# Performance work log

Hardware: AMD Instinct MI355X
Metric: run time of the kernel (lower is better)

Reference implementation:

```python
import jax, jax.numpy as jnp
import numpy as np
from jax import lax

NUM_STEPS = 32
NUM_CLASSES = 10
HIDDEN = 1024


def setup_inputs() -> dict:
    key = jax.random.key(0)
    ks = jax.random.split(key, 4)
    B, H, W, C = 8, 1024, 2048, 4
    x = jax.random.normal(ks[0], (B, H, W, C), dtype=jnp.float32)
    conv_w = jax.random.normal(ks[1], (C,), dtype=jnp.float32) * 0.5
    conv_b = jnp.zeros((1,), dtype=jnp.float32)
    w1 = jax.random.normal(ks[2], (HIDDEN, W), dtype=jnp.float32) * (1.0 / np.sqrt(W))
    b1 = jnp.zeros((HIDDEN,), dtype=jnp.float32)
    w2 = jax.random.normal(ks[3], (NUM_CLASSES, HIDDEN), dtype=jnp.float32) * (1.0 / np.sqrt(HIDDEN))
    b2 = jnp.zeros((NUM_CLASSES,), dtype=jnp.float32)
    beta1 = jnp.full((1,), 0.95, dtype=jnp.float32)
    thr1 = jnp.ones((1,), dtype=jnp.float32)
    beta2 = jnp.full((1,), 0.95, dtype=jnp.float32)
    thr2 = jnp.ones((1,), dtype=jnp.float32)
    return {"x": x, "conv_w": conv_w, "conv_b": conv_b, "w1": w1, "b1": b1,
            "beta1": beta1, "thr1": thr1, "w2": w2, "b2": b2,
            "beta2": beta2, "thr2": thr2}


def _leaky_scan(inp_t, beta, thr):
    # inp_t: [T, ...]; snntorch Leaky, reset_mechanism='subtract', reset_delay=False
    b = jnp.clip(beta, 0.0, 1.0)

    def step(mem, u):
        mem = b * mem + u
        spk = (mem > thr).astype(u.dtype)   # heaviside spike
        mem = mem - spk * thr               # subtract reset (no delay)
        return mem, spk

    mem0 = jnp.zeros(inp_t.shape[1:], dtype=inp_t.dtype)
    _, spks = lax.scan(step, mem0, inp_t)
    return spks  # [T, ...]


def reference(x, conv_w, conv_b, w1, b1, beta1, thr1, w2, b2, beta2, thr2):
    # x: [B, H, W, 4]; 1x1 conv over 4 antenna channels -> 1 channel
    xf = jnp.einsum('bhwc,c->bhw', x, conv_w) + conv_b[0]       # [B, H, W]
    B, H, W = xf.shape
    G = H // NUM_STEPS
    xr = xf.reshape(B, G, NUM_STEPS, W)                          # [B, G, T, 2048]
    h = jnp.einsum('bgtw,dw->bgtd', xr, w1) + b1                 # [B, G, T, D]
    spks1 = _leaky_scan(jnp.moveaxis(h, 2, 0), beta1, thr1)      # [T, B, G, D]
    s = spks1.sum(axis=0)                                        # [B, G, D]
    h2 = jnp.einsum('bgd,cd->bgc', s, w2) + b2                   # [B, G, C]
    spks2 = _leaky_scan(jnp.moveaxis(h2, 1, 0), beta2, thr2)     # [G, B, C]
    logits = spks2.sum(axis=0)                                   # [B, C]
    return jax.nn.softmax(logits, axis=1)
```

## Files before the change

kernel.cpp:

```cpp
#include <hip/hip_runtime.h>

#define TSTEPS 32
#define HID 1024
#define NCLS 10
#define BATCH 8
#define GGRP 32
#define MROWS 8192
#define GK 2048
#define GN 1024
#define BUFSH 24576

typedef __attribute__((ext_vector_type(8))) short bf16x8;
typedef __attribute__((ext_vector_type(16))) float f32x16;

__device__ __forceinline__ unsigned short bf16_rne(float v) {
    unsigned u = __builtin_bit_cast(unsigned, v);
    return (unsigned short)((u + 0x7FFFu + ((u >> 16) & 1u)) >> 16);
}
__device__ __forceinline__ float bf16_f(unsigned short h) {
    unsigned u = (unsigned)h << 16;
    return __builtin_bit_cast(float, u);
}
__device__ __forceinline__ void gload16(const unsigned short* g, unsigned short* l) {
    __builtin_amdgcn_global_load_lds(
        (const __attribute__((address_space(1))) void*)g,
        (__attribute__((address_space(3))) void*)l, 16, 0, 0);
}


__global__ __launch_bounds__(256) void conv_pack_kernel(
    const float4* __restrict__ x, const float* __restrict__ cw,
    const float* __restrict__ cb,
    unsigned short* __restrict__ Ahi, unsigned short* __restrict__ Alo)
{
    const int rb = blockIdx.x >> 6;
    const int kb = blockIdx.x & 63;
    const float c0 = cw[0], c1 = cw[1], c2 = cw[2], c3 = cw[3], cbv = cb[0];
    const int tid = threadIdx.x;
#pragma unroll
    for (int cc = 0; cc < 2; ++cc) {
        int c = tid + cc * 256;
        int u = c >> 6, w = c & 63;
        int row = (u >> 1) * 32 + (w & 31);
        int k0  = (u & 1) * 16 + (w >> 5) * 8;
        const float4* px = x + ((size_t)(rb * 128 + row) * 2048 + kb * 32 + k0);
        bf16x8 h8, l8;
#pragma unroll
        for (int e = 0; e < 8; ++e) {
            float4 a = px[e];
            float v = a.x * c0 + a.y * c1 + a.z * c2 + a.w * c3 + cbv;
            unsigned short h = bf16_rne(v);
            h8[e] = (short)h;
            l8[e] = (short)bf16_rne(v - bf16_f(h));
        }
        size_t off = ((size_t)blockIdx.x * 512 + c) * 8;
        *(bf16x8*)(Ahi + off) = h8;
        *(bf16x8*)(Alo + off) = l8;
    }
}

__global__ __launch_bounds__(256) void wpack_kernel(
    const float* __restrict__ wsrc, unsigned short* __restrict__ Bhi,
    unsigned short* __restrict__ Blo)
{
    const int kb  = blockIdx.x & 63;
    const int cbk = blockIdx.x >> 6;
    const int tid = threadIdx.x;
#pragma unroll
    for (int cc = 0; cc < 4; ++cc) {
        int c = tid + cc * 256;
        int u = c >> 6, w = c & 63;
        int col = cbk * 256 + (u >> 1) * 32 + (w & 31);
        int k0  = kb * 32 + (u & 1) * 16 + (w >> 5) * 8;
        const float* pw = wsrc + ((size_t)col * 2048 + k0);
        bf16x8 h8, l8;
#pragma unroll
        for (int e = 0; e < 8; ++e) {
            float v = pw[e];
            unsigned short h = bf16_rne(v);
            h8[e] = (short)h;
            l8[e] = (short)bf16_rne(v - bf16_f(h));
        }
        size_t off = ((size_t)blockIdx.x * 1024 + c) * 8;
        *(bf16x8*)(Bhi + off) = h8;
        *(bf16x8*)(Blo + off) = l8;
    }
}

__global__ __launch_bounds__(512) void gemm_scan_kernel(
    const unsigned short* __restrict__ Ahi, const unsigned short* __restrict__ Alo,
    const unsigned short* __restrict__ Bhi, const unsigned short* __restrict__ Blo,
    const float* __restrict__ bias,
    const float* __restrict__ beta1, const float* __restrict__ thr1,
    float* __restrict__ S)
{
    __shared__ __align__(16) unsigned short sm[3 * BUFSH];

    const int tid = threadIdx.x;
    const int lane = tid & 63, wv = tid >> 6;
    const int wr = wv >> 2, wc = wv & 3;
    const int by = blockIdx.x & 63;
    const int bx = blockIdx.x >> 6;

    const unsigned short* gAh = Ahi + (size_t)by * 262144;
    const unsigned short* gAl = Alo + (size_t)by * 262144;
    const unsigned short* gBh = Bhi + (size_t)bx * 524288;
    const unsigned short* gBl = Blo + (size_t)bx * 524288;

    f32x16 acc[2][2];
#pragma unroll
    for (int i = 0; i < 2; ++i)
#pragma unroll
        for (int j = 0; j < 2; ++j) acc[i][j] = (f32x16)0.f;

#define STAGE(buf, kb_)                                                          \
    {                                                                            \
        unsigned short* dst = sm + (buf) * BUFSH;                                \
        const size_t ao = (size_t)(kb_) * 4096 + tid * 8;                        \
        const size_t bo = (size_t)(kb_) * 8192 + tid * 8;                        \
        gload16(gAh + ao, dst + tid * 8);                                        \
        gload16(gAl + ao, dst + 4096 + tid * 8);                                 \
        gload16(gBh + bo, dst + 8192 + tid * 8);                                 \
        gload16(gBh + bo + 4096, dst + 12288 + tid * 8);                         \
        gload16(gBl + bo, dst + 16384 + tid * 8);                                \
        gload16(gBl + bo + 4096, dst + 20480 + tid * 8);                         \
    }

    STAGE(0, 0);
    STAGE(1, 1);

    const int fo = ((lane & 31) + 32 * (lane >> 5)) * 8;

    int cur = 0;
    for (int kb = 0; kb < 64; ++kb) {
        if (kb < 63) asm volatile("s_waitcnt vmcnt(6)" ::: "memory");
        else         asm volatile("s_waitcnt vmcnt(0)" ::: "memory");
        __builtin_amdgcn_s_barrier();

        int nbuf = cur + 2; if (nbuf >= 3) nbuf -= 3;
        if (kb < 62) STAGE(nbuf, kb + 2);

        const unsigned short* bufp = sm + cur * BUFSH;
        bf16x8 ah[2][2], al[2][2], bh[2][2], bl[2][2];
#pragma unroll
        for (int i = 0; i < 2; ++i)
#pragma unroll
            for (int kh = 0; kh < 2; ++kh) {
                int ua = (((wr * 2 + i) * 2 + kh) << 9) + fo;
                ah[i][kh] = *(const bf16x8*)(bufp + ua);
                al[i][kh] = *(const bf16x8*)(bufp + 4096 + ua);
            }
#pragma unroll
        for (int j = 0; j < 2; ++j)
#pragma unroll
            for (int kh = 0; kh < 2; ++kh) {
                int ub = (((wc * 2 + j) * 2 + kh) << 9) + fo;
                bh[j][kh] = *(const bf16x8*)(bufp + 8192 + ub);
                bl[j][kh] = *(const bf16x8*)(bufp + 16384 + ub);
            }
#pragma unroll
        for (int kh = 0; kh < 2; ++kh) {
#pragma unroll
            for (int i = 0; i < 2; ++i)
#pragma unroll
                for (int j = 0; j < 2; ++j)
                    acc[i][j] = __builtin_amdgcn_mfma_f32_32x32x16_bf16(ah[i][kh], bh[j][kh], acc[i][j], 0, 0, 0);
#pragma unroll
            for (int i = 0; i < 2; ++i)
#pragma unroll
                for (int j = 0; j < 2; ++j)
                    acc[i][j] = __builtin_amdgcn_mfma_f32_32x32x16_bf16(ah[i][kh], bl[j][kh], acc[i][j], 0, 0, 0);
#pragma unroll
            for (int i = 0; i < 2; ++i)
#pragma unroll
                for (int j = 0; j < 2; ++j)
                    acc[i][j] = __builtin_amdgcn_mfma_f32_32x32x16_bf16(al[i][kh], bh[j][kh], acc[i][j], 0, 0, 0);
        }
        cur = (cur == 2) ? 0 : cur + 1;
    }
    __syncthreads();

    float* sb = (float*)sm;
    const float bclamp = fminf(fmaxf(beta1[0], 0.f), 1.f);
    const float th = thr1[0];
    const int sbg = tid >> 8;
    const int scol = tid & 255;
    const float bv = bias[bx * 256 + scol];

#pragma unroll
    for (int band = 0; band < 2; ++band) {
        if (wr == band) {
#pragma unroll
            for (int i = 0; i < 2; ++i)
#pragma unroll
                for (int j = 0; j < 2; ++j)
#pragma unroll
                    for (int r = 0; r < 16; ++r) {
                        int lr = i * 32 + (r & 3) + 8 * (r >> 2) + 4 * (lane >> 5);
                        int lc = wc * 64 + j * 32 + (lane & 31);
                        sb[lr * 256 + lc] = acc[i][j][r];
                    }
        }
        __syncthreads();
        float mem = 0.f, cnt = 0.f;
#pragma unroll
        for (int t = 0; t < TSTEPS; ++t) {
            float u = sb[(sbg * 32 + t) * 256 + scol] + bv;
            mem = bclamp * mem + u;
            float spk = mem > th ? 1.f : 0.f;
            mem -= spk * th;
            cnt += spk;
        }
        int bgg = by * 4 + band * 2 + sbg;
        S[(size_t)bgg * GN + bx * 256 + scol] = cnt;
        __syncthreads();
    }
}

__global__ __launch_bounds__(256) void fc2_kernel(
    const float* __restrict__ s, const float* __restrict__ w2,
    const float* __restrict__ b2, float* __restrict__ h2)
{
    int bg  = blockIdx.x;
    int tid = threadIdx.x;
    const float* sp = s + (size_t)bg * HID;
    float part[NCLS];
#pragma unroll
    for (int c = 0; c < NCLS; ++c) part[c] = 0.f;
    for (int d = tid; d < HID; d += 256) {
        float sv = sp[d];
#pragma unroll
        for (int c = 0; c < NCLS; ++c) part[c] += sv * w2[c * HID + d];
    }
#pragma unroll
    for (int c = 0; c < NCLS; ++c)
        for (int off = 32; off > 0; off >>= 1)
            part[c] += __shfl_down(part[c], off, 64);
    __shared__ float red[NCLS][4];
    int wave = tid >> 6, lanei = tid & 63;
    if (lanei == 0)
#pragma unroll
        for (int c = 0; c < NCLS; ++c) red[c][wave] = part[c];
    __syncthreads();
    if (tid < NCLS) {
        float v = red[tid][0] + red[tid][1] + red[tid][2] + red[tid][3] + b2[tid];
        h2[bg * NCLS + tid] = v;
    }
}

__global__ __launch_bounds__(128) void scan2_kernel(
    const float* __restrict__ h2, const float* __restrict__ beta2,
    const float* __restrict__ thr2, float* __restrict__ out)
{
    __shared__ float logits[BATCH][NCLS];
    int t = threadIdx.x;
    if (t < BATCH * NCLS) {
        int b = t / NCLS, c = t % NCLS;
        float bb = fminf(fmaxf(beta2[0], 0.f), 1.f);
        float th = thr2[0];
        float mem = 0.f, lg = 0.f;
        for (int g = 0; g < GGRP; ++g) {
            float u = h2[(b * GGRP + g) * NCLS + c];
            mem = bb * mem + u;
            float spk = mem > th ? 1.f : 0.f;
            mem -= spk * th;
            lg += spk;
        }
        logits[b][c] = lg;
    }
    __syncthreads();
    if (t < BATCH) {
        float mx = -1e30f;
        for (int c = 0; c < NCLS; ++c) mx = fmaxf(mx, logits[t][c]);
        float e[NCLS];
        float sum = 0.f;
        for (int c = 0; c < NCLS; ++c) { e[c] = expf(logits[t][c] - mx); sum += e[c]; }
        for (int c = 0; c < NCLS; ++c) out[t * NCLS + c] = e[c] / sum;
    }
}

extern "C" void kernel_launch(void* const* d_in, const int* in_sizes, int n_in,
                              void* d_out, int out_size, void* d_ws, size_t ws_size,
                              hipStream_t stream)
{
    const float* x     = (const float*)d_in[0];
    const float* cw    = (const float*)d_in[1];
    const float* cb    = (const float*)d_in[2];
    const float* w1    = (const float*)d_in[3];
    const float* b1    = (const float*)d_in[4];
    const float* beta1 = (const float*)d_in[5];
    const float* thr1  = (const float*)d_in[6];
    const float* w2    = (const float*)d_in[7];
    const float* b2    = (const float*)d_in[8];
    const float* beta2 = (const float*)d_in[9];
    const float* thr2  = (const float*)d_in[10];
    float* out = (float*)d_out;

    unsigned short* ahi = (unsigned short*)d_ws;
    unsigned short* alo = ahi + (size_t)MROWS * GK;
    unsigned short* bhi = alo + (size_t)MROWS * GK;
    unsigned short* blo = bhi + (size_t)GN * GK;
    float* s  = (float*)(blo + (size_t)GN * GK);
    float* h2 = s + (size_t)BATCH * GGRP * HID;

    conv_pack_kernel<<<4096, 256, 0, stream>>>((const float4*)x, cw, cb, ahi, alo);
    wpack_kernel    <<<256, 256, 0, stream>>>(w1, bhi, blo);
    gemm_scan_kernel<<<256, 512, 0, stream>>>(ahi, alo, bhi, blo, b1, beta1, thr1, s);
    fc2_kernel      <<<256, 256, 0, stream>>>(s, w2, b2, h2);
    scan2_kernel    <<<1, 128, 0, stream>>>(h2, beta2, thr2, out);
}
```

Baseline: 171.6 us.

## Coalesce conv-pack loads via LDS and software-pipeline GEMM fragment reads

The conv/pack kernel now reads x with coalesced float4 loads, so consecutive threads read consecutive pixels. It converts the values to bf16 hi/lo pairs in a padded LDS tile and then writes the packed fragments from LDS, replacing the old per-thread strided 8-pixel loads. In the GEMM kernel the main loop is unrolled by two, with double-buffered register fragments. LDS reads for the next k-block are issued before the MFMAs of the current one, and the prologue prefetches three stages. This is meant to hide LDS latency behind MFMA work and cut DRAM inefficiency in the bandwidth-bound conv stage, at the cost of more registers and extra LDS in the pack kernel.

```diff
diff --git a/kernel.cpp b/kernel.cpp
--- a/kernel.cpp
+++ b/kernel.cpp
@@ -9,6 +9,7 @@
 #define GK 2048
 #define GN 1024
 #define BUFSH 24576
+#define CLDS 40
 
 typedef __attribute__((ext_vector_type(8))) short bf16x8;
 typedef __attribute__((ext_vector_type(16))) float f32x16;
@@ -33,26 +34,33 @@
     const float* __restrict__ cb,
     unsigned short* __restrict__ Ahi, unsigned short* __restrict__ Alo)
 {
+    __shared__ __align__(16) unsigned short lh[128 * CLDS];
+    __shared__ __align__(16) unsigned short ll[128 * CLDS];
     const int rb = blockIdx.x >> 6;
     const int kb = blockIdx.x & 63;
     const float c0 = cw[0], c1 = cw[1], c2 = cw[2], c3 = cw[3], cbv = cb[0];
     const int tid = threadIdx.x;
+
+#pragma unroll
+    for (int p = 0; p < 16; ++p) {
+        int i = p * 256 + tid;
+        int row = i >> 5, px = i & 31;
+        float4 a = x[(size_t)(rb * 128 + row) * 2048 + kb * 32 + px];
+        float v = a.x * c0 + a.y * c1 + a.z * c2 + a.w * c3 + cbv;
+        unsigned short h = bf16_rne(v);
+        lh[row * CLDS + px] = h;
+        ll[row * CLDS + px] = bf16_rne(v - bf16_f(h));
+    }
+    __syncthreads();
+
 #pragma unroll
     for (int cc = 0; cc < 2; ++cc) {
         int c = tid + cc * 256;
         int u = c >> 6, w = c & 63;
         int row = (u >> 1) * 32 + (w & 31);
-        int k0  = (u & 1) * 16 + (w >> 5) * 8;
-        const float4* px = x + ((size_t)(rb * 128 + row) * 2048 + kb * 32 + k0);
-        bf16x8 h8, l8;
-#pragma unroll
-        for (int e = 0; e < 8; ++e) {
-            float4 a = px[e];
-            float v = a.x * c0 + a.y * c1 + a.z * c2 + a.w * c3 + cbv;
-            unsigned short h = bf16_rne(v);
-            h8[e] = (short)h;
-            l8[e] = (short)bf16_rne(v - bf16_f(h));
-        }
+        int ko  = (u & 1) * 2 + (w >> 5);
+        bf16x8 h8 = *(const bf16x8*)(lh + row * CLDS + ko * 8);
+        bf16x8 l8 = *(const bf16x8*)(ll + row * CLDS + ko * 8);
         size_t off = ((size_t)blockIdx.x * 512 + c) * 8;
         *(bf16x8*)(Ahi + off) = h8;
         *(bf16x8*)(Alo + off) = l8;
@@ -112,6 +120,8 @@
     for (int i = 0; i < 2; ++i)
 #pragma unroll
         for (int j = 0; j < 2; ++j) acc[i][j] = (f32x16)0.f;
+
+    bf16x8 fr[2][16];
 
 #define STAGE(buf, kb_)                                                          \
     {                                                                            \
@@ -126,58 +136,83 @@
         gload16(gBl + bo + 4096, dst + 20480 + tid * 8);                         \
     }
 
+#define READF(s, bufp)                                                           \
+    {                                                                            \
+        const unsigned short* bp_ = (bufp);                                      \
+        _Pragma("unroll")                                                        \
+        for (int i = 0; i < 2; ++i)                                              \
+            _Pragma("unroll")                                                    \
+            for (int kh = 0; kh < 2; ++kh) {                                     \
+                int ua = (((wr * 2 + i) * 2 + kh) << 9) + fo;                    \
+                fr[s][(i * 2 + kh) * 2 + 0] = *(const bf16x8*)(bp_ + ua);        \
+                fr[s][(i * 2 + kh) * 2 + 1] = *(const bf16x8*)(bp_ + 4096 + ua); \
+            }                                                                    \
+        _Pragma("unroll")                                                        \
+        for (int j = 0; j < 2; ++j)                                              \
+            _Pragma("unroll")                                                    \
+            for (int kh = 0; kh < 2; ++kh) {                                     \
+                int ub = (((wc * 2 + j) * 2 + kh) << 9) + fo;                    \
+                fr[s][8 + (j * 2 + kh) * 2 + 0] = *(const bf16x8*)(bp_ + 8192 + ub);  \
+                fr[s][8 + (j * 2 + kh) * 2 + 1] = *(const bf16x8*)(bp_ + 16384 + ub); \
+            }                                                                    \
+    }
+
+#define MFMAF(s)                                                                 \
+    {                                                                            \
+        _Pragma("unroll")                                                        \
+        for (int kh = 0; kh < 2; ++kh) {                                         \
+            _Pragma("unroll")                                                    \
+            for (int i = 0; i < 2; ++i)                                          \
+                _Pragma("unroll")                                                \
+                for (int j = 0; j < 2; ++j)                                      \
+                    acc[i][j] = __builtin_amdgcn_mfma_f32_32x32x16_bf16(         \
+                        fr[s][(i * 2 + kh) * 2], fr[s][8 + (j * 2 + kh) * 2],    \
+                        acc[i][j], 0, 0, 0);                                     \
+            _Pragma("unroll")                                                    \
+            for (int i = 0; i < 2; ++i)                                          \
+                _Pragma("unroll")                                                \
+                for (int j = 0; j < 2; ++j)                                      \
+                    acc[i][j] = __builtin_amdgcn_mfma_f32_32x32x16_bf16(         \
+                        fr[s][(i * 2 + kh) * 2], fr[s][8 + (j * 2 + kh) * 2 + 1],\
+                        acc[i][j], 0, 0, 0);                                     \
+            _Pragma("unroll")                                                    \
+            for (int i = 0; i < 2; ++i)                                          \
+                _Pragma("unroll")                                                \
+                for (int j = 0; j < 2; ++j)                                      \
+                    acc[i][j] = __builtin_amdgcn_mfma_f32_32x32x16_bf16(         \
+                        fr[s][(i * 2 + kh) * 2 + 1], fr[s][8 + (j * 2 + kh) * 2],\
+                        acc[i][j], 0, 0, 0);                                     \
+        }                                                                        \
+    }
+
+#define KSTEP(SC, SN, KB)                                                        \
+    {                                                                            \
+        if ((KB) < 63) asm volatile("s_waitcnt vmcnt(6)" ::: "memory");          \
+        else           asm volatile("s_waitcnt vmcnt(0)" ::: "memory");          \
+        asm volatile("s_waitcnt lgkmcnt(0)" ::: "memory");                       \
+        __builtin_amdgcn_sched_barrier(0);                                       \
+        __builtin_amdgcn_s_barrier();                                            \
+        if ((KB) <= 61) STAGE(((KB) + 2) % 3, (KB) + 2);                         \
+        READF(SN, sm + ((KB) % 3) * BUFSH);                                      \
+        MFMAF(SC);                                                               \
+    }
+
     STAGE(0, 0);
     STAGE(1, 1);
-
+    STAGE(2, 2);
+    asm volatile("s_waitcnt vmcnt(12)" ::: "memory");
+    __builtin_amdgcn_s_barrier();
     const int fo = ((lane & 31) + 32 * (lane >> 5)) * 8;
-
-    int cur = 0;
-    for (int kb = 0; kb < 64; ++kb) {
-        if (kb < 63) asm volatile("s_waitcnt vmcnt(6)" ::: "memory");
-        else         asm volatile("s_waitcnt vmcnt(0)" ::: "memory");
-        __builtin_amdgcn_s_barrier();
-
-        int nbuf = cur + 2; if (nbuf >= 3) nbuf -= 3;
-        if (kb < 62) STAGE(nbuf, kb + 2);
-
-        const unsigned short* bufp = sm + cur * BUFSH;
-        bf16x8 ah[2][2], al[2][2], bh[2][2], bl[2][2];
-#pragma unroll
-        for (int i = 0; i < 2; ++i)
-#pragma unroll
-            for (int kh = 0; kh < 2; ++kh) {
-                int ua = (((wr * 2 + i) * 2 + kh) << 9) + fo;
-                ah[i][kh] = *(const bf16x8*)(bufp + ua);
-                al[i][kh] = *(const bf16x8*)(bufp + 4096 + ua);
-            }
-#pragma unroll
-        for (int j = 0; j < 2; ++j)
-#pragma unroll
-            for (int kh = 0; kh < 2; ++kh) {
-                int ub = (((wc * 2 + j) * 2 + kh) << 9) + fo;
-                bh[j][kh] = *(const bf16x8*)(bufp + 8192 + ub);
-                bl[j][kh] = *(const bf16x8*)(bufp + 16384 + ub);
-            }
-#pragma unroll
-        for (int kh = 0; kh < 2; ++kh) {
-#pragma unroll
-            for (int i = 0; i < 2; ++i)
-#pragma unroll
-                for (int j = 0; j < 2; ++j)
-                    acc[i][j] = __builtin_amdgcn_mfma_f32_32x32x16_bf16(ah[i][kh], bh[j][kh], acc[i][j], 0, 0, 0);
-#pragma unroll
-            for (int i = 0; i < 2; ++i)
-#pragma unroll
-                for (int j = 0; j < 2; ++j)
-                    acc[i][j] = __builtin_amdgcn_mfma_f32_32x32x16_bf16(ah[i][kh], bl[j][kh], acc[i][j], 0, 0, 0);
-#pragma unroll
-            for (int i = 0; i < 2; ++i)
-#pragma unroll
-                for (int j = 0; j < 2; ++j)
-                    acc[i][j] = __builtin_amdgcn_mfma_f32_32x32x16_bf16(al[i][kh], bh[j][kh], acc[i][j], 0, 0, 0);
-        }
-        cur = (cur == 2) ? 0 : cur + 1;
-    }
+    READF(0, sm);
+
+    for (int kb = 1; kb < 63; kb += 2) {
+        KSTEP(0, 1, kb);
+        KSTEP(1, 0, kb + 1);
+    }
+    KSTEP(0, 1, 63);
+    asm volatile("s_waitcnt lgkmcnt(0)" ::: "memory");
+    __builtin_amdgcn_sched_barrier(0);
+    MFMAF(1);
     __syncthreads();
 
     float* sb = (float*)sm;
```

After: 154.9 us. -9.7%, faster.
